# Optimization experiments

Measured on AMD Instinct MI355X. Metric: run time of the kernel, lower is better.

## Reference

```python
import jax, jax.numpy as jnp
import numpy as np
import math

B, C, H, W = 64, 32, 80, 80
HEADS, HD = 8, 4
L = H * W
INV_PI = 1.0 / math.pi


def _conv2d(x, w, pad):
    return jax.lax.conv_general_dilated(x, w, (1, 1), pad, dimension_numbers=('NCHW', 'OIHW', 'NCHW'))


def _lin_angular(x, qkv_w, proj_w, proj_b, dconv_w):
    # x: (B, L, C) -> softmax-free angular linear attention
    qkv = (x @ qkv_w.T).reshape(B, L, 3, HEADS, HD).transpose(2, 0, 3, 1, 4)
    q, k, v = qkv[0], qkv[1], qkv[2]  # (B, HEADS, L, HD)
    q = q / jnp.linalg.norm(q, axis=-1, keepdims=True)
    k = k / jnp.linalg.norm(k, axis=-1, keepdims=True)
    # depthwise conv over L with kernel (9,1), one channel per head
    dconv_v = jax.lax.conv_general_dilated(v, dconv_w, (1, 1), ((4, 4), (0, 0)),
                                           feature_group_count=HEADS,
                                           dimension_numbers=('NCHW', 'OIHW', 'NCHW'))
    attn = jnp.einsum('bhld,bhle->bhde', k, v)  # (B,H,HD,HD)
    out = 0.5 * v + INV_PI * jnp.einsum('bhld,bhde->bhle', q, attn)
    out = out / jnp.linalg.norm(out, axis=-1, keepdims=True)
    out = out + dconv_v
    out = out.transpose(0, 2, 1, 3).reshape(B, L, C)
    return out @ proj_w.T + proj_b


def _xca(x, qkv_w, temp, proj_w, proj_b):
    # x: (B, L, C) -> cross-covariance (channel) attention
    qkv = (x @ qkv_w.T).reshape(B, L, 3, HEADS, HD).transpose(2, 0, 3, 4, 1)
    q, k, v = qkv[0], qkv[1], qkv[2]  # (B, HEADS, HD, L)
    q = q / jnp.maximum(jnp.linalg.norm(q, axis=-1, keepdims=True), 1e-12)
    k = k / jnp.maximum(jnp.linalg.norm(k, axis=-1, keepdims=True), 1e-12)
    attn = jax.nn.softmax(jnp.einsum('bhdn,bhen->bhde', q, k) * temp, axis=-1)
    out = jnp.einsum('bhde,bhen->bhdn', attn, v)  # (B,H,HD,L)
    out = out.transpose(0, 3, 1, 2).reshape(B, L, C)
    return out @ proj_w.T + proj_b


def _chan_vec(f, wa, ba, wa2, ba2, wm, bm, wm2, bm2):
    # f: (B, C, L) -> (B, C, 1) pooled channel descriptor (avg + max branches)
    avg = f.mean(axis=-1)  # (B, C)
    mx = f.max(axis=-1)    # (B, C)
    a = jax.nn.relu(avg @ wa.T + ba) @ wa2.T + ba2
    m = jax.nn.relu(mx @ wm.T + bm) @ wm2.T + bm2
    return (a + m)[..., None]  # (B, C, 1)


def _spatial_gate(a, c1w, c1b, c2w, c2b):
    # a: (B, C, L) -> (B, 1, L) softmax spatial gate
    am = a.reshape(B, C, H, W)
    pooled = jnp.concatenate([am.mean(axis=1, keepdims=True), am.max(axis=1, keepdims=True)], axis=1)
    y = jax.nn.relu(_conv2d(pooled, c1w, ((1, 1), (1, 1))) + c1b[None, :, None, None])
    y = _conv2d(y, c2w, ((1, 1), (1, 1))) + c2b[None, :, None, None]
    return jax.nn.softmax(y.reshape(B, 1, L), axis=-1)


def _forward(rgb, freq, la_qkv_w, la_proj_w, la_proj_b, la_dconv_w,
             xa_qkv_w, xa_temp, xa_proj_w, xa_proj_b,
             c1s_w, c1s_b, c2s_w, c2s_b,
             avg1_w, avg1_b, max1_w, max1_b, avg2_w, avg2_b, max2_w, max2_b,
             avg11_w, avg11_b, max11_w, max11_b, avg22_w, avg22_b, max22_w, max22_b):
    x1 = rgb.reshape(B, C, L).transpose(0, 2, 1)  # to_3d: (B, L, C)
    la1 = _lin_angular(x1, la_qkv_w, la_proj_w, la_proj_b, la_dconv_w)
    x2 = freq.reshape(B, C, L).transpose(0, 2, 1)
    xa1 = _xca(x2, xa_qkv_w, xa_temp, xa_proj_w, xa_proj_b)
    # CAFM works on flattened (B, C, L)
    f1 = la1.transpose(0, 2, 1)
    f2 = xa1.transpose(0, 2, 1)
    a1 = _chan_vec(f1, avg1_w, avg1_b, avg11_w, avg11_b, max1_w, max1_b, max11_w, max11_b)
    a2 = _chan_vec(f2, avg2_w, avg2_b, avg22_w, avg22_b, max2_w, max2_b, max22_w, max22_b)
    cross = jnp.einsum('bci,bdi->bcd', a1, a2)  # (B, C, C)
    a1f = jnp.einsum('bcd,bdl->bcl', jax.nn.softmax(cross, axis=-1), f1)
    a2f = jnp.einsum('bcd,bdl->bcl', jax.nn.softmax(cross.transpose(0, 2, 1), axis=-1), f2)
    g1 = _spatial_gate(a1f, c1s_w, c1s_b, c2s_w, c2s_b)
    g2 = _spatial_gate(a2f, c1s_w, c1s_b, c2s_w, c2s_b)
    f1 = f1 * g1 + f1
    f2 = f2 * g2 + f2
    # torch: (B,C,L).transpose(0,1) -> (C,B,L); sum; permute(1,2,0) -> (B,L,C); to_4d -> (B,C,H,W)
    # transposes cancel: equivalent to (f1+f2).reshape(B, C, H, W)
    return (f1 + f2).reshape(B, C, H, W)


def setup_inputs() -> dict:
    key = jax.random.key(0)
    ks = iter(jax.random.split(key, 40))
    def rn(shape, s=0.05):
        return jax.random.normal(next(ks), shape, dtype=jnp.float32) * s
    return dict(
        rgb=jax.random.normal(next(ks), (B, C, H, W), dtype=jnp.float32),
        freq=jax.random.normal(next(ks), (B, C, H, W), dtype=jnp.float32),
        la_qkv_w=rn((3 * C, C)), la_proj_w=rn((C, C)), la_proj_b=jnp.zeros((C,), jnp.float32),
        la_dconv_w=rn((HEADS, 1, 9, 1)),
        xa_qkv_w=rn((3 * C, C)), xa_temp=jnp.ones((HEADS, 1, 1), jnp.float32),
        xa_proj_w=rn((C, C)), xa_proj_b=jnp.zeros((C,), jnp.float32),
        c1s_w=rn((1, 2, 3, 3)), c1s_b=jnp.zeros((1,), jnp.float32),
        c2s_w=rn((1, 1, 3, 3)), c2s_b=jnp.zeros((1,), jnp.float32),
        avg1_w=rn((16, C)), avg1_b=jnp.zeros((16,), jnp.float32),
        max1_w=rn((16, C)), max1_b=jnp.zeros((16,), jnp.float32),
        avg2_w=rn((16, C)), avg2_b=jnp.zeros((16,), jnp.float32),
        max2_w=rn((16, C)), max2_b=jnp.zeros((16,), jnp.float32),
        avg11_w=rn((C, 16)), avg11_b=jnp.zeros((C,), jnp.float32),
        max11_w=rn((C, 16)), max11_b=jnp.zeros((C,), jnp.float32),
        avg22_w=rn((C, 16)), avg22_b=jnp.zeros((C,), jnp.float32),
        max22_w=rn((C, 16)), max22_b=jnp.zeros((C,), jnp.float32),
    )


def reference(rgb, freq, la_qkv_w, la_proj_w, la_proj_b, la_dconv_w,
              xa_qkv_w, xa_temp, xa_proj_w, xa_proj_b,
              c1s_w, c1s_b, c2s_w, c2s_b,
              avg1_w, avg1_b, max1_w, max1_b, avg2_w, avg2_b, max2_w, max2_b,
              avg11_w, avg11_b, max11_w, max11_b, avg22_w, avg22_b, max22_w, max22_b):
    return _forward(rgb, freq, la_qkv_w, la_proj_w, la_proj_b, la_dconv_w,
                    xa_qkv_w, xa_temp, xa_proj_w, xa_proj_b,
                    c1s_w, c1s_b, c2s_w, c2s_b,
                    avg1_w, avg1_b, max1_w, max1_b, avg2_w, avg2_b, max2_w, max2_b,
                    avg11_w, avg11_b, max11_w, max11_b, avg22_w, avg22_b, max22_w, max22_b)
```

## Files before the change

### kernel.cpp

```cpp
#include <hip/hip_runtime.h>

#define BN 64
#define CN 32
#define HEADSN 8
#define HDN 4
#define LN 6400
#define CL (CN*LN)


__device__ __forceinline__ unsigned fenc(float f){
  unsigned u = __float_as_uint(f);
  return (u & 0x80000000u) ? ~u : (u | 0x80000000u);
}
__device__ __forceinline__ float fdec(unsigned u){
  unsigned v = (u & 0x80000000u) ? (u & 0x7FFFFFFFu) : ~u;
  return __uint_as_float(v);
}

__device__ __forceinline__ unsigned pk_bf16(float a, float b){
  unsigned ua = __float_as_uint(a), ub = __float_as_uint(b);
  ua = (ua + 0x7fffu + ((ua >> 16) & 1u)) >> 16;
  ub = (ub + 0x7fffu + ((ub >> 16) & 1u)) >> 16;
  return ua | (ub << 16);
}
__device__ __forceinline__ float2 upk_bf16(unsigned u){
  return make_float2(__uint_as_float(u << 16), __uint_as_float(u & 0xffff0000u));
}

template<bool MAXOP>
__device__ __forceinline__ float bfly32(const float* in, int lane, int* chOut){
  const bool h0 = (lane & 1)  != 0, h1 = (lane & 2)  != 0, h2 = (lane & 4) != 0,
             h3 = (lane & 8)  != 0, h4 = (lane & 16) != 0;
  float a[16];
  #pragma unroll
  for (int i = 0; i < 16; ++i){
    float send = h0 ? in[i] : in[i+16];
    float keep = h0 ? in[i+16] : in[i];
    float recv = __shfl_xor(send, 1, 64);
    a[i] = MAXOP ? fmaxf(keep, recv) : keep + recv;
  }
  float b[8];
  #pragma unroll
  for (int i = 0; i < 8; ++i){
    float send = h1 ? a[i] : a[i+8];
    float keep = h1 ? a[i+8] : a[i];
    float recv = __shfl_xor(send, 2, 64);
    b[i] = MAXOP ? fmaxf(keep, recv) : keep + recv;
  }
  float c[4];
  #pragma unroll
  for (int i = 0; i < 4; ++i){
    float send = h2 ? b[i] : b[i+4];
    float keep = h2 ? b[i+4] : b[i];
    float recv = __shfl_xor(send, 4, 64);
    c[i] = MAXOP ? fmaxf(keep, recv) : keep + recv;
  }
  float d[2];
  #pragma unroll
  for (int i = 0; i < 2; ++i){
    float send = h3 ? c[i] : c[i+2];
    float keep = h3 ? c[i+2] : c[i];
    float recv = __shfl_xor(send, 8, 64);
    d[i] = MAXOP ? fmaxf(keep, recv) : keep + recv;
  }
  float e;
  {
    float send = h4 ? d[0] : d[1];
    float keep = h4 ? d[1] : d[0];
    float recv = __shfl_xor(send, 16, 64);
    e = MAXOP ? fmaxf(keep, recv) : keep + recv;
  }
  {
    float recv = __shfl_xor(e, 32, 64);
    e = MAXOP ? fmaxf(e, recv) : e + recv;
  }
  *chOut = (h0?16:0)|(h1?8:0)|(h2?4:0)|(h3?2:0)|(h4?1:0);
  return e;
}

__device__ __forceinline__ float bfly16_sum(const float* in, int lane, int* chOut){
  const bool h0 = (lane & 1) != 0, h1 = (lane & 2) != 0, h2 = (lane & 4) != 0,
             h3 = (lane & 8) != 0;
  float a[8];
  #pragma unroll
  for (int i = 0; i < 8; ++i){
    float send = h0 ? in[i] : in[i+8];
    float keep = h0 ? in[i+8] : in[i];
    float recv = __shfl_xor(send, 1, 64);
    a[i] = keep + recv;
  }
  float b[4];
  #pragma unroll
  for (int i = 0; i < 4; ++i){
    float send = h1 ? a[i] : a[i+4];
    float keep = h1 ? a[i+4] : a[i];
    float recv = __shfl_xor(send, 2, 64);
    b[i] = keep + recv;
  }
  float c[2];
  #pragma unroll
  for (int i = 0; i < 2; ++i){
    float send = h2 ? b[i] : b[i+2];
    float keep = h2 ? b[i+2] : b[i];
    float recv = __shfl_xor(send, 4, 64);
    c[i] = keep + recv;
  }
  float e;
  {
    float send = h3 ? c[0] : c[1];
    float keep = h3 ? c[1] : c[0];
    float recv = __shfl_xor(send, 8, 64);
    e = keep + recv;
  }
  e += __shfl_xor(e, 16, 64);
  e += __shfl_xor(e, 32, 64);
  *chOut = (h0?8:0)|(h1?4:0)|(h2?2:0)|(h3?1:0);
  return e;
}

__global__ __launch_bounds__(256) void k_reduce2(const float* __restrict__ rgb,
    const float* __restrict__ freq, const float* __restrict__ Wla,
    const float* __restrict__ Wxa, float* __restrict__ la_attn,
    float* __restrict__ xa_sums){
  __shared__ float2 xs2[256*17];
  const bool isXA = blockIdx.x >= 25;
  const int b = blockIdx.y, tid = threadIdx.x;
  const int l0 = (isXA ? (int)blockIdx.x - 25 : (int)blockIdx.x)*256;
  const float* xg = (isXA ? freq : rgb) + (size_t)b*CL + l0;
  #pragma unroll
  for (int c2 = 0; c2 < 16; ++c2){
    float e0 = xg[(2*c2)*LN + tid];
    float e1 = xg[(2*c2+1)*LN + tid];
    xs2[tid*17 + c2] = make_float2(e0, e1);
  }
  __syncthreads();
  const int wave = __builtin_amdgcn_readfirstlane(tid >> 6);
  const int lane = tid & 63;
  if (!isXA){
    const float* Wk = Wla + (32 + wave*8)*32;
    const float* Wv = Wla + (64 + wave*8)*32;
    float acc[32];
    #pragma unroll
    for (int i = 0; i < 32; ++i) acc[i] = 0.f;
    for (int it = 0; it < 4; ++it){
      const int ll = it*64 + lane;
      float xv[32];
      #pragma unroll
      for (int c2 = 0; c2 < 16; ++c2){
        float2 t = xs2[ll*17 + c2];
        xv[2*c2] = t.x; xv[2*c2+1] = t.y;
      }
      float kk[8], vv[8];
      #pragma unroll
      for (int r = 0; r < 8; ++r){ kk[r] = 0.f; vv[r] = 0.f; }
      #pragma unroll
      for (int c = 0; c < 32; ++c){
        #pragma unroll
        for (int r = 0; r < 8; ++r){
          kk[r] = fmaf(Wk[r*32 + c], xv[c], kk[r]);
          vv[r] = fmaf(Wv[r*32 + c], xv[c], vv[r]);
        }
      }
      #pragma unroll
      for (int hh = 0; hh < 2; ++hh){
        const float* k = kk + hh*4;
        const float* v = vv + hh*4;
        float rn = rsqrtf(k[0]*k[0] + k[1]*k[1] + k[2]*k[2] + k[3]*k[3]);
        #pragma unroll
        for (int d = 0; d < 4; ++d){
          float kn = k[d]*rn;
          #pragma unroll
          for (int e = 0; e < 4; ++e)
            acc[hh*16 + d*4 + e] = fmaf(kn, v[e], acc[hh*16 + d*4 + e]);
        }
      }
    }
    int ch;
    float s = bfly32<false>(acc, lane, &ch);
    if (lane < 32) atomicAdd(la_attn + b*128 + wave*32 + ch, s);
  } else {
    const float* Wq = Wxa + (0  + wave*8)*32;
    const float* Wk = Wxa + (32 + wave*8)*32;
    float acc[48];
    #pragma unroll
    for (int i = 0; i < 48; ++i) acc[i] = 0.f;
    for (int it = 0; it < 4; ++it){
      const int ll = it*64 + lane;
      float xv[32];
      #pragma unroll
      for (int c2 = 0; c2 < 16; ++c2){
        float2 t = xs2[ll*17 + c2];
        xv[2*c2] = t.x; xv[2*c2+1] = t.y;
      }
      float qq[8], kk[8];
      #pragma unroll
      for (int r = 0; r < 8; ++r){ qq[r] = 0.f; kk[r] = 0.f; }
      #pragma unroll
      for (int c = 0; c < 32; ++c){
        #pragma unroll
        for (int r = 0; r < 8; ++r){
          qq[r] = fmaf(Wq[r*32 + c], xv[c], qq[r]);
          kk[r] = fmaf(Wk[r*32 + c], xv[c], kk[r]);
        }
      }
      #pragma unroll
      for (int hh = 0; hh < 2; ++hh){
        const float* q = qq + hh*4;
        const float* k = kk + hh*4;
        const int base = hh*24;
        #pragma unroll
        for (int d = 0; d < 4; ++d){
          #pragma unroll
          for (int e = 0; e < 4; ++e)
            acc[base + d*4 + e] = fmaf(q[d], k[e], acc[base + d*4 + e]);
        }
        #pragma unroll
        for (int d = 0; d < 4; ++d) acc[base + 16 + d] = fmaf(q[d], q[d], acc[base + 16 + d]);
        #pragma unroll
        for (int e = 0; e < 4; ++e) acc[base + 20 + e] = fmaf(k[e], k[e], acc[base + 20 + e]);
      }
    }
    float* dst = xa_sums + b*192 + wave*48;
    int ch;
    float s0 = bfly32<false>(acc, lane, &ch);
    if (lane < 32) atomicAdd(dst + ch, s0);
    int ch2;
    float s1 = bfly16_sum(acc + 32, lane, &ch2);
    if (lane < 16) atomicAdd(dst + 32 + ch2, s1);
  }
}

__global__ __launch_bounds__(64) void k_fold(const float* __restrict__ xa_sums,
                                             const float* __restrict__ temp,
                                             const float* __restrict__ Wqkv,
                                             const float* __restrict__ Wp,
                                             float* __restrict__ M2){
  __shared__ float attn_s[128];
  const int b = blockIdx.x, t = threadIdx.x;
  if (t < 32){
    const int h = t >> 2, d = t & 3;
    const float* xss = xa_sums + b*192 + h*24;
    const float tmp = temp[h];
    const float nq = fmaxf(sqrtf(xss[16 + d]), 1e-12f);
    float lg[4]; float m = -1e30f;
    #pragma unroll
    for (int e = 0; e < 4; ++e){
      float nk = fmaxf(sqrtf(xss[20 + e]), 1e-12f);
      lg[e] = xss[d*4 + e] * tmp / (nq*nk);
      m = fmaxf(m, lg[e]);
    }
    float Z = 0.f;
    #pragma unroll
    for (int e = 0; e < 4; ++e){ lg[e] = __expf(lg[e] - m); Z += lg[e]; }
    float iZ = 1.f/Z;
    #pragma unroll
    for (int e = 0; e < 4; ++e) attn_s[h*16 + d*4 + e] = lg[e]*iZ;
  }
  __syncthreads();
  if (t < 32){
    const int c = t;
    const float* Wv = Wqkv + 64*32;
    float tmpv[32];
    #pragma unroll
    for (int k = 0; k < 32; ++k){
      const int h = k >> 2, d = k & 3;
      float s = 0.f;
      #pragma unroll
      for (int e = 0; e < 4; ++e)
        s = fmaf(attn_s[h*16 + d*4 + e], Wv[(h*4 + e)*32 + c], s);
      tmpv[k] = s;
    }
    float out[32];
    #pragma unroll
    for (int r = 0; r < 32; ++r) out[r] = 0.f;
    #pragma unroll
    for (int k = 0; k < 32; ++k){
      #pragma unroll
      for (int r = 0; r < 32; ++r)
        out[r] = fmaf(Wp[r*32 + k], tmpv[k], out[r]);
    }
    #pragma unroll
    for (int r = 0; r < 32; ++r) M2[b*1024 + r*32 + c] = out[r];
  }
}

__global__ __launch_bounds__(256) void k_finalize2(const float* __restrict__ rgb,
    const float* __restrict__ freq, const float* __restrict__ Wqkv,
    const float* __restrict__ la_attn, const float* __restrict__ dconv_w,
    const float* __restrict__ Wp, const float* __restrict__ bp,
    const float* __restrict__ M2, const float* __restrict__ xbp,
    float* __restrict__ f1, float* __restrict__ sum1, unsigned* __restrict__ max1e,
    float* __restrict__ f2, float* __restrict__ sum2, unsigned* __restrict__ max2e){
  __shared__ unsigned vsh[264*17];
  const bool isXA = blockIdx.x >= 25;
  const int b = blockIdx.y, tid = threadIdx.x;
  const int l0 = (isXA ? (int)blockIdx.x - 25 : (int)blockIdx.x)*256;
  const int l = l0 + tid, lane = tid & 63;
  if (!isXA){
    const float* xg = rgb + (size_t)b*CL;
    float x[32];
    #pragma unroll
    for (int c = 0; c < 32; ++c) x[c] = xg[c*LN + l];
    {
      float v[32];
      #pragma unroll
      for (int r = 0; r < 32; ++r) v[r] = 0.f;
      const float* Wv = Wqkv + 64*32;
      #pragma unroll
      for (int c = 0; c < 32; ++c){
        #pragma unroll
        for (int r = 0; r < 32; ++r) v[r] = fmaf(Wv[r*32 + c], x[c], v[r]);
      }
      #pragma unroll
      for (int c2 = 0; c2 < 16; ++c2)
        vsh[(tid+4)*17 + c2] = pk_bf16(v[2*c2], v[2*c2+1]);
    }
    if (tid < 128){
      const int p = tid >> 4, c2 = tid & 15;
      const int hl  = (p < 4) ? (l0 - 4 + p) : (l0 + 252 + p);
      const int pos = (p < 4) ? p : (256 + p);
      float2 vh = make_float2(0.f, 0.f);
      if (hl >= 0 && hl < LN){
        const float* W0 = Wqkv + (64 + 2*c2)*32;
        #pragma unroll 8
        for (int cc = 0; cc < 32; ++cc){
          float xv = xg[cc*LN + hl];
          vh.x = fmaf(W0[cc],      xv, vh.x);
          vh.y = fmaf(W0[32 + cc], xv, vh.y);
        }
      }
      vsh[pos*17 + c2] = pk_bf16(vh.x, vh.y);
    }
    __syncthreads();
    float y[32];
    #pragma unroll
    for (int h = 0; h < 8; ++h){
      float q0 = 0.f, q1 = 0.f, q2 = 0.f, q3 = 0.f;
      const float* Wq = Wqkv + h*4*32;
      #pragma unroll
      for (int c = 0; c < 32; ++c){
        q0 = fmaf(Wq[c],      x[c], q0);
        q1 = fmaf(Wq[32 + c], x[c], q1);
        q2 = fmaf(Wq[64 + c], x[c], q2);
        q3 = fmaf(Wq[96 + c], x[c], q3);
      }
      const float rnq = rsqrtf(q0*q0 + q1*q1 + q2*q2 + q3*q3);
      q0 *= rnq; q1 *= rnq; q2 *= rnq; q3 *= rnq;
      const float* at = la_attn + b*128 + h*16;
      const float2 v01 = upk_bf16(vsh[(tid+4)*17 + h*2]);
      const float2 v23 = upk_bf16(vsh[(tid+4)*17 + h*2 + 1]);
      const float vo[4] = {v01.x, v01.y, v23.x, v23.y};
      float o[4]; float ss = 0.f;
      #pragma unroll
      for (int e = 0; e < 4; ++e){
        float t = 0.f;
        t = fmaf(q0, at[e],      t);
        t = fmaf(q1, at[4 + e],  t);
        t = fmaf(q2, at[8 + e],  t);
        t = fmaf(q3, at[12 + e], t);
        o[e] = fmaf(0.31830988618379067f, t, 0.5f*vo[e]);
        ss = fmaf(o[e], o[e], ss);
      }
      const float rno = rsqrtf(ss);
      float dc[4] = {0.f, 0.f, 0.f, 0.f};
      #pragma unroll
      for (int j = 0; j < 9; ++j){
        const float w = dconv_w[h*9 + j];
        const float2 p0 = upk_bf16(vsh[(tid + j)*17 + h*2]);
        const float2 p1 = upk_bf16(vsh[(tid + j)*17 + h*2 + 1]);
        dc[0] = fmaf(w, p0.x, dc[0]);
        dc[1] = fmaf(w, p0.y, dc[1]);
        dc[2] = fmaf(w, p1.x, dc[2]);
        dc[3] = fmaf(w, p1.y, dc[3]);
      }
      #pragma unroll
      for (int e = 0; e < 4; ++e) y[h*4 + e] = fmaf(o[e], rno, dc[e]);
    }
    float vals[32];
    float* f1p = f1 + (size_t)b*CL + l;
    #pragma unroll
    for (int r = 0; r < 32; ++r){
      float val = bp[r];
      #pragma unroll
      for (int c = 0; c < 32; ++c) val = fmaf(Wp[r*32 + c], y[c], val);
      f1p[r*LN] = val;
      vals[r] = val;
    }
    int ch;
    float s = bfly32<false>(vals, lane, &ch);
    float m = bfly32<true >(vals, lane, &ch);
    if (lane < 32){
      atomicAdd(&sum1[b*32 + ch], s);
      atomicMax(&max1e[b*32 + ch], fenc(m));
    }
  } else {
    const float* xg = freq + (size_t)b*CL;
    float x[32];
    #pragma unroll
    for (int c = 0; c < 32; ++c) x[c] = xg[c*LN + l];
    const float* M = M2 + b*1024;
    float vals[32];
    #pragma unroll
    for (int r = 0; r < 32; ++r) vals[r] = xbp[r];
    #pragma unroll
    for (int c = 0; c < 32; ++c){
      #pragma unroll
      for (int r = 0; r < 32; ++r) vals[r] = fmaf(M[r*32 + c], x[c], vals[r]);
    }
    float* f2p = f2 + (size_t)b*CL + l;
    #pragma unroll
    for (int r = 0; r < 32; ++r) f2p[r*LN] = vals[r];
    int ch;
    float s = bfly32<false>(vals, lane, &ch);
    float m = bfly32<true >(vals, lane, &ch);
    if (lane < 32){
      atomicAdd(&sum2[b*32 + ch], s);
      atomicMax(&max2e[b*32 + ch], fenc(m));
    }
  }
}

__global__ __launch_bounds__(64) void k_vec(
  const float* __restrict__ sum1, const unsigned* __restrict__ max1e,
  const float* __restrict__ sum2, const unsigned* __restrict__ max2e,
  const float* __restrict__ a1w, const float* __restrict__ a1b,
  const float* __restrict__ m1w, const float* __restrict__ m1b,
  const float* __restrict__ a2w, const float* __restrict__ a2b,
  const float* __restrict__ m2w, const float* __restrict__ m2b,
  const float* __restrict__ a11w, const float* __restrict__ a11b,
  const float* __restrict__ m11w, const float* __restrict__ m11b,
  const float* __restrict__ a22w, const float* __restrict__ a22b,
  const float* __restrict__ m22w, const float* __restrict__ m22b,
  float* __restrict__ w1o, float* __restrict__ w2o){
  __shared__ float avg1[32], mx1[32], avg2[32], mx2[32];
  __shared__ float h_a1[16], h_m1[16], h_a2[16], h_m2[16];
  __shared__ float a1v[32], a2v[32];
  const int b = blockIdx.x, t = threadIdx.x;
  if (t < 32){
    avg1[t] = sum1[b*32 + t] * (1.f/6400.f);
    mx1[t]  = fdec(max1e[b*32 + t]);
    avg2[t] = sum2[b*32 + t] * (1.f/6400.f);
    mx2[t]  = fdec(max2e[b*32 + t]);
  }
  __syncthreads();
  if (t < 16){
    float s1 = a1b[t], s2 = m1b[t], s3 = a2b[t], s4 = m2b[t];
    for (int c = 0; c < 32; ++c){
      s1 = fmaf(avg1[c], a1w[t*32 + c], s1);
      s2 = fmaf(mx1[c],  m1w[t*32 + c], s2);
      s3 = fmaf(avg2[c], a2w[t*32 + c], s3);
      s4 = fmaf(mx2[c],  m2w[t*32 + c], s4);
    }
    h_a1[t] = fmaxf(s1, 0.f); h_m1[t] = fmaxf(s2, 0.f);
    h_a2[t] = fmaxf(s3, 0.f); h_m2[t] = fmaxf(s4, 0.f);
  }
  __syncthreads();
  if (t < 32){
    float v1 = a11b[t] + m11b[t];
    float v2 = a22b[t] + m22b[t];
    for (int k = 0; k < 16; ++k){
      v1 += h_a1[k]*a11w[t*16 + k] + h_m1[k]*m11w[t*16 + k];
      v2 += h_a2[k]*a22w[t*16 + k] + h_m2[k]*m22w[t*16 + k];
    }
    a1v[t] = v1; a2v[t] = v2;
  }
  __syncthreads();
  if (t < 32){
    float s = a1v[t], m = -1e30f;
    for (int d = 0; d < 32; ++d) m = fmaxf(m, s*a2v[d]);
    float Z = 0.f;
    for (int d = 0; d < 32; ++d) Z += __expf(s*a2v[d] - m);
    float iZ = 1.f/Z;
    for (int d = 0; d < 32; ++d) w1o[b*1024 + t*32 + d] = __expf(s*a2v[d] - m)*iZ;
    float s2 = a2v[t]; m = -1e30f;
    for (int d = 0; d < 32; ++d) m = fmaxf(m, s2*a1v[d]);
    Z = 0.f;
    for (int d = 0; d < 32; ++d) Z += __expf(s2*a1v[d] - m);
    iZ = 1.f/Z;
    for (int d = 0; d < 32; ++d) w2o[b*1024 + t*32 + d] = __expf(s2*a1v[d] - m)*iZ;
  }
}

__global__ __launch_bounds__(256) void k_mix(const float* __restrict__ f1,
    const float* __restrict__ f2, const float* __restrict__ w1,
    const float* __restrict__ w2, float* __restrict__ pooled1,
    float* __restrict__ pooled2){
  const int b = blockIdx.y, l = blockIdx.x*256 + threadIdx.x;
  float fv[32], av[32];
  {
    const float* f1p = f1 + (size_t)b*CL + l;
    #pragma unroll
    for (int d = 0; d < 32; ++d) fv[d] = f1p[d*LN];
    const float* W = w1 + b*1024;
    #pragma unroll
    for (int c = 0; c < 32; ++c) av[c] = 0.f;
    #pragma unroll
    for (int d = 0; d < 32; ++d){
      #pragma unroll
      for (int c = 0; c < 32; ++c) av[c] = fmaf(W[c*32 + d], fv[d], av[c]);
    }
    float s = 0.f, m = -1e30f;
    #pragma unroll
    for (int c = 0; c < 32; ++c){ s += av[c]; m = fmaxf(m, av[c]); }
    pooled1[(size_t)b*2*LN + l]      = s*(1.f/32.f);
    pooled1[(size_t)b*2*LN + LN + l] = m;
  }
  {
    const float* f2p = f2 + (size_t)b*CL + l;
    #pragma unroll
    for (int d = 0; d < 32; ++d) fv[d] = f2p[d*LN];
    const float* W = w2 + b*1024;
    #pragma unroll
    for (int c = 0; c < 32; ++c) av[c] = 0.f;
    #pragma unroll
    for (int d = 0; d < 32; ++d){
      #pragma unroll
      for (int c = 0; c < 32; ++c) av[c] = fmaf(W[c*32 + d], fv[d], av[c]);
    }
    float s = 0.f, m = -1e30f;
    #pragma unroll
    for (int c = 0; c < 32; ++c){ s += av[c]; m = fmaxf(m, av[c]); }
    pooled2[(size_t)b*2*LN + l]      = s*(1.f/32.f);
    pooled2[(size_t)b*2*LN + LN + l] = m;
  }
}

__global__ __launch_bounds__(256) void k_gate(const float* __restrict__ pooled1,
    const float* __restrict__ pooled2, const float* __restrict__ c1w,
    const float* __restrict__ c1b, const float* __restrict__ c2w,
    const float* __restrict__ c2b, float* __restrict__ g1, float* __restrict__ g2){
  __shared__ float y1s[6400];
  __shared__ float red[8];
  const int b = blockIdx.y, t = blockIdx.x, tid = threadIdx.x;
  const float* src = (t == 0 ? pooled1 : pooled2) + (size_t)b*2*LN;
  float* dst = (t == 0 ? g1 : g2) + (size_t)b*LN;
  for (int i = tid; i < 6400; i += 256){
    const int yy = i/80, xx = i - yy*80;
    float a = c1b[0];
    #pragma unroll
    for (int ky = 0; ky < 3; ++ky){
      const int y2 = yy + ky - 1;
      if (y2 < 0 || y2 >= 80) continue;
      #pragma unroll
      for (int kx = 0; kx < 3; ++kx){
        const int x2 = xx + kx - 1;
        if (x2 < 0 || x2 >= 80) continue;
        const int j = y2*80 + x2;
        a = fmaf(src[j],        c1w[ky*3 + kx],     a);
        a = fmaf(src[6400 + j], c1w[9 + ky*3 + kx], a);
      }
    }
    y1s[i] = fmaxf(a, 0.f);
  }
  __syncthreads();
  float y2r[25]; float lmax = -1e30f;
  #pragma unroll
  for (int ii = 0; ii < 25; ++ii){
    const int i = tid + ii*256;
    const int yy = i/80, xx = i - yy*80;
    float a = c2b[0];
    #pragma unroll
    for (int ky = 0; ky < 3; ++ky){
      const int y2 = yy + ky - 1;
      if (y2 < 0 || y2 >= 80) continue;
      #pragma unroll
      for (int kx = 0; kx < 3; ++kx){
        const int x2 = xx + kx - 1;
        if (x2 < 0 || x2 >= 80) continue;
        a = fmaf(y1s[y2*80 + x2], c2w[ky*3 + kx], a);
      }
    }
    y2r[ii] = a; lmax = fmaxf(lmax, a);
  }
  #pragma unroll
  for (int off = 32; off >= 1; off >>= 1) lmax = fmaxf(lmax, __shfl_xor(lmax, off, 64));
  if ((tid & 63) == 0) red[tid >> 6] = lmax;
  __syncthreads();
  const float bmax = fmaxf(fmaxf(red[0], red[1]), fmaxf(red[2], red[3]));
  float lsum = 0.f;
  #pragma unroll
  for (int ii = 0; ii < 25; ++ii){
    float e = __expf(y2r[ii] - bmax);
    y2r[ii] = e; lsum += e;
  }
  #pragma unroll
  for (int off = 32; off >= 1; off >>= 1) lsum += __shfl_xor(lsum, off, 64);
  if ((tid & 63) == 0) red[4 + (tid >> 6)] = lsum;
  __syncthreads();
  const float inv = 1.f/(red[4] + red[5] + red[6] + red[7]);
  #pragma unroll
  for (int ii = 0; ii < 25; ++ii) dst[tid + ii*256] = y2r[ii]*inv;
}

__global__ __launch_bounds__(256) void k_final(const float* __restrict__ f1,
    const float* __restrict__ f2, const float* __restrict__ g1,
    const float* __restrict__ g2, float* __restrict__ out){
  const int i = blockIdx.x*256 + threadIdx.x;
  const int flat = i*4;
  const int b = flat / CL;
  const int rem = flat - b*CL;
  const int l = rem % LN;
  const float4 a  = *(const float4*)(f1 + flat);
  const float4 c  = *(const float4*)(f2 + flat);
  const float4 ga = *(const float4*)(g1 + b*LN + l);
  const float4 gc = *(const float4*)(g2 + b*LN + l);
  float4 o;
  o.x = fmaf(a.x, ga.x, a.x) + fmaf(c.x, gc.x, c.x);
  o.y = fmaf(a.y, ga.y, a.y) + fmaf(c.y, gc.y, c.y);
  o.z = fmaf(a.z, ga.z, a.z) + fmaf(c.z, gc.z, c.z);
  o.w = fmaf(a.w, ga.w, a.w) + fmaf(c.w, gc.w, c.w);
  *(float4*)(out + flat) = o;
}

extern "C" void kernel_launch(void* const* d_in, const int* in_sizes, int n_in,
                              void* d_out, int out_size, void* d_ws, size_t ws_size,
                              hipStream_t stream){
  const float* rgb     = (const float*)d_in[0];
  const float* freq    = (const float*)d_in[1];
  const float* la_qkv  = (const float*)d_in[2];
  const float* la_pw   = (const float*)d_in[3];
  const float* la_pb   = (const float*)d_in[4];
  const float* la_dw   = (const float*)d_in[5];
  const float* xa_qkv  = (const float*)d_in[6];
  const float* xa_temp = (const float*)d_in[7];
  const float* xa_pw   = (const float*)d_in[8];
  const float* xa_pb   = (const float*)d_in[9];
  const float* c1w     = (const float*)d_in[10];
  const float* c1b     = (const float*)d_in[11];
  const float* c2w     = (const float*)d_in[12];
  const float* c2b     = (const float*)d_in[13];

  float* ws = (float*)d_ws;
  size_t o = 0;
  float* f1      = ws + o; o += (size_t)BN*CL;
  float* f2      = ws + o; o += (size_t)BN*CL;
  float* la_attn = ws + o; o += BN*128;
  float* xa_sums = ws + o; o += BN*192;
  float* sum1    = ws + o; o += BN*32;
  unsigned* max1e = (unsigned*)(ws + o); o += BN*32;
  float* sum2    = ws + o; o += BN*32;
  unsigned* max2e = (unsigned*)(ws + o); o += BN*32;
  float* w1      = ws + o; o += BN*1024;
  float* w2      = ws + o; o += BN*1024;
  float* pooled1 = ws + o; o += (size_t)BN*2*LN;
  float* pooled2 = ws + o; o += (size_t)BN*2*LN;
  float* g1      = ws + o; o += (size_t)BN*LN;
  float* g2      = ws + o; o += (size_t)BN*LN;
  float* M2      = ws + o; o += (size_t)BN*1024;

  const size_t nz = (size_t)BN*128 + BN*192 + (size_t)BN*32*4;
  hipMemsetAsync(la_attn, 0, nz*sizeof(float), stream);

  k_reduce2<<<dim3(50, BN), 256, 0, stream>>>(rgb, freq, la_qkv, xa_qkv, la_attn, xa_sums);
  k_fold   <<<BN, 64, 0, stream>>>(xa_sums, xa_temp, xa_qkv, xa_pw, M2);
  k_finalize2<<<dim3(50, BN), 256, 0, stream>>>(rgb, freq, la_qkv, la_attn, la_dw,
                                                la_pw, la_pb, M2, xa_pb,
                                                f1, sum1, max1e, f2, sum2, max2e);
  k_vec<<<BN, 64, 0, stream>>>(sum1, max1e, sum2, max2e,
      (const float*)d_in[14], (const float*)d_in[15], (const float*)d_in[16], (const float*)d_in[17],
      (const float*)d_in[18], (const float*)d_in[19], (const float*)d_in[20], (const float*)d_in[21],
      (const float*)d_in[22], (const float*)d_in[23], (const float*)d_in[24], (const float*)d_in[25],
      (const float*)d_in[26], (const float*)d_in[27], (const float*)d_in[28], (const float*)d_in[29],
      w1, w2);
  k_mix  <<<dim3(25, BN), 256, 0, stream>>>(f1, f2, w1, w2, pooled1, pooled2);
  k_gate <<<dim3(2, BN), 256, 0, stream>>>(pooled1, pooled2, c1w, c1b, c2w, c2b, g1, g2);
  k_final<<<12800, 256, 0, stream>>>(f1, f2, g1, g2, (float*)d_out);
}
```

Measured before the change: 537.5 us.

## Fuse fold and channel-vector kernels into consumers; use 512-thread blocks

Folds the small k_fold work (XCA softmax and the M2 projection matrix) into the XCA blocks of k_finalize2. It also folds k_vec's channel-weight computation into each k_mix block, keeping the weights in shared memory. This removes two tiny launches and their global round-trips. k_reduce2 and k_finalize2 move to 512-thread blocks that each handle two tiles. The trade-off is redundant per-block recomputation of the fold and vector work: every XCA finalize block and every mix block recomputes its batch's matrices serially on 32 threads, which adds latency before the main work starts.

```diff
diff --git a/kernel.cpp b/kernel.cpp
--- a/kernel.cpp
+++ b/kernel.cpp
@@ -118,23 +118,32 @@
   return e;
 }
 
-__global__ __launch_bounds__(256) void k_reduce2(const float* __restrict__ rgb,
+__global__ __launch_bounds__(512) void k_reduce2(const float* __restrict__ rgb,
     const float* __restrict__ freq, const float* __restrict__ Wla,
     const float* __restrict__ Wxa, float* __restrict__ la_attn,
     float* __restrict__ xa_sums){
-  __shared__ float2 xs2[256*17];
+  __shared__ float2 xs2[2*128*17];
   const bool isXA = blockIdx.x >= 25;
   const int b = blockIdx.y, tid = threadIdx.x;
-  const int l0 = (isXA ? (int)blockIdx.x - 25 : (int)blockIdx.x)*256;
+  const int half = tid >> 8;
+  const int wt = tid & 255;
+  const int bxt = isXA ? (int)blockIdx.x - 25 : (int)blockIdx.x;
+  const int l0 = (bxt*2 + half)*128;
   const float* xg = (isXA ? freq : rgb) + (size_t)b*CL + l0;
-  #pragma unroll
-  for (int c2 = 0; c2 < 16; ++c2){
-    float e0 = xg[(2*c2)*LN + tid];
-    float e1 = xg[(2*c2+1)*LN + tid];
-    xs2[tid*17 + c2] = make_float2(e0, e1);
-  }
-  __syncthreads();
-  const int wave = __builtin_amdgcn_readfirstlane(tid >> 6);
+  float2* xs = xs2 + half*(128*17);
+  {
+    const int px = wt & 127;
+    const int c2b_ = (wt >> 7)*8;
+    #pragma unroll
+    for (int j = 0; j < 8; ++j){
+      const int c2 = c2b_ + j;
+      float e0 = xg[(2*c2)*LN + px];
+      float e1 = xg[(2*c2+1)*LN + px];
+      xs[px*17 + c2] = make_float2(e0, e1);
+    }
+  }
+  __syncthreads();
+  const int wave = __builtin_amdgcn_readfirstlane((tid >> 6) & 3);
   const int lane = tid & 63;
   if (!isXA){
     const float* Wk = Wla + (32 + wave*8)*32;
@@ -142,12 +151,12 @@
     float acc[32];
     #pragma unroll
     for (int i = 0; i < 32; ++i) acc[i] = 0.f;
-    for (int it = 0; it < 4; ++it){
+    for (int it = 0; it < 2; ++it){
       const int ll = it*64 + lane;
       float xv[32];
       #pragma unroll
       for (int c2 = 0; c2 < 16; ++c2){
-        float2 t = xs2[ll*17 + c2];
+        float2 t = xs[ll*17 + c2];
         xv[2*c2] = t.x; xv[2*c2+1] = t.y;
       }
       float kk[8], vv[8];
@@ -184,12 +193,12 @@
     float acc[48];
     #pragma unroll
     for (int i = 0; i < 48; ++i) acc[i] = 0.f;
-    for (int it = 0; it < 4; ++it){
+    for (int it = 0; it < 2; ++it){
       const int ll = it*64 + lane;
       float xv[32];
       #pragma unroll
       for (int c2 = 0; c2 < 16; ++c2){
-        float2 t = xs2[ll*17 + c2];
+        float2 t = xs[ll*17 + c2];
         xv[2*c2] = t.x; xv[2*c2+1] = t.y;
       }
       float qq[8], kk[8];
@@ -230,274 +239,276 @@
   }
 }
 
-__global__ __launch_bounds__(64) void k_fold(const float* __restrict__ xa_sums,
-                                             const float* __restrict__ temp,
-                                             const float* __restrict__ Wqkv,
-                                             const float* __restrict__ Wp,
-                                             float* __restrict__ M2){
-  __shared__ float attn_s[128];
-  const int b = blockIdx.x, t = threadIdx.x;
-  if (t < 32){
-    const int h = t >> 2, d = t & 3;
-    const float* xss = xa_sums + b*192 + h*24;
-    const float tmp = temp[h];
-    const float nq = fmaxf(sqrtf(xss[16 + d]), 1e-12f);
-    float lg[4]; float m = -1e30f;
-    #pragma unroll
-    for (int e = 0; e < 4; ++e){
-      float nk = fmaxf(sqrtf(xss[20 + e]), 1e-12f);
-      lg[e] = xss[d*4 + e] * tmp / (nq*nk);
-      m = fmaxf(m, lg[e]);
-    }
-    float Z = 0.f;
-    #pragma unroll
-    for (int e = 0; e < 4; ++e){ lg[e] = __expf(lg[e] - m); Z += lg[e]; }
-    float iZ = 1.f/Z;
-    #pragma unroll
-    for (int e = 0; e < 4; ++e) attn_s[h*16 + d*4 + e] = lg[e]*iZ;
-  }
-  __syncthreads();
-  if (t < 32){
-    const int c = t;
-    const float* Wv = Wqkv + 64*32;
-    float tmpv[32];
-    #pragma unroll
-    for (int k = 0; k < 32; ++k){
-      const int h = k >> 2, d = k & 3;
-      float s = 0.f;
-      #pragma unroll
-      for (int e = 0; e < 4; ++e)
-        s = fmaf(attn_s[h*16 + d*4 + e], Wv[(h*4 + e)*32 + c], s);
-      tmpv[k] = s;
-    }
-    float out[32];
-    #pragma unroll
-    for (int r = 0; r < 32; ++r) out[r] = 0.f;
-    #pragma unroll
-    for (int k = 0; k < 32; ++k){
-      #pragma unroll
-      for (int r = 0; r < 32; ++r)
-        out[r] = fmaf(Wp[r*32 + k], tmpv[k], out[r]);
-    }
-    #pragma unroll
-    for (int r = 0; r < 32; ++r) M2[b*1024 + r*32 + c] = out[r];
-  }
-}
-
-__global__ __launch_bounds__(256) void k_finalize2(const float* __restrict__ rgb,
+__global__ __launch_bounds__(512) void k_finalize2(const float* __restrict__ rgb,
     const float* __restrict__ freq, const float* __restrict__ Wqkv,
     const float* __restrict__ la_attn, const float* __restrict__ dconv_w,
     const float* __restrict__ Wp, const float* __restrict__ bp,
-    const float* __restrict__ M2, const float* __restrict__ xbp,
+    const float* __restrict__ Wxa, const float* __restrict__ xtemp,
+    const float* __restrict__ xWp, const float* __restrict__ xbp,
+    const float* __restrict__ xa_sums,
     float* __restrict__ f1, float* __restrict__ sum1, unsigned* __restrict__ max1e,
     float* __restrict__ f2, float* __restrict__ sum2, unsigned* __restrict__ max2e){
-  __shared__ unsigned vsh[264*17];
-  const bool isXA = blockIdx.x >= 25;
+  __shared__ unsigned vsh[2*264*17];
+  const bool isXA = blockIdx.x >= 13;
   const int b = blockIdx.y, tid = threadIdx.x;
-  const int l0 = (isXA ? (int)blockIdx.x - 25 : (int)blockIdx.x)*256;
-  const int l = l0 + tid, lane = tid & 63;
+  const int half = tid >> 8, t = tid & 255;
+  const int bxt = isXA ? (int)blockIdx.x - 13 : (int)blockIdx.x;
+  const int tile = bxt*2 + half;
+  const bool valid = tile < 25;
+  const int l0 = tile*256;
+  const int l = l0 + t, lane = tid & 63;
+  unsigned* vs = vsh + half*(264*17);
   if (!isXA){
     const float* xg = rgb + (size_t)b*CL;
     float x[32];
-    #pragma unroll
-    for (int c = 0; c < 32; ++c) x[c] = xg[c*LN + l];
-    {
-      float v[32];
-      #pragma unroll
-      for (int r = 0; r < 32; ++r) v[r] = 0.f;
-      const float* Wv = Wqkv + 64*32;
+    if (valid){
+      #pragma unroll
+      for (int c = 0; c < 32; ++c) x[c] = xg[c*LN + l];
+      {
+        float v[32];
+        #pragma unroll
+        for (int r = 0; r < 32; ++r) v[r] = 0.f;
+        const float* Wv = Wqkv + 64*32;
+        #pragma unroll
+        for (int c = 0; c < 32; ++c){
+          #pragma unroll
+          for (int r = 0; r < 32; ++r) v[r] = fmaf(Wv[r*32 + c], x[c], v[r]);
+        }
+        #pragma unroll
+        for (int c2 = 0; c2 < 16; ++c2)
+          vs[(t+4)*17 + c2] = pk_bf16(v[2*c2], v[2*c2+1]);
+      }
+      if (t < 128){
+        const int p = t >> 4, c2 = t & 15;
+        const int hl  = (p < 4) ? (l0 - 4 + p) : (l0 + 252 + p);
+        const int pos = (p < 4) ? p : (256 + p);
+        float2 vh = make_float2(0.f, 0.f);
+        if (hl >= 0 && hl < LN){
+          const float* W0 = Wqkv + (64 + 2*c2)*32;
+          #pragma unroll 8
+          for (int cc = 0; cc < 32; ++cc){
+            float xv = xg[cc*LN + hl];
+            vh.x = fmaf(W0[cc],      xv, vh.x);
+            vh.y = fmaf(W0[32 + cc], xv, vh.y);
+          }
+        }
+        vs[pos*17 + c2] = pk_bf16(vh.x, vh.y);
+      }
+    }
+    __syncthreads();
+    if (valid){
+      float y[32];
+      #pragma unroll
+      for (int h = 0; h < 8; ++h){
+        float q0 = 0.f, q1 = 0.f, q2 = 0.f, q3 = 0.f;
+        const float* Wq = Wqkv + h*4*32;
+        #pragma unroll
+        for (int c = 0; c < 32; ++c){
+          q0 = fmaf(Wq[c],      x[c], q0);
+          q1 = fmaf(Wq[32 + c], x[c], q1);
+          q2 = fmaf(Wq[64 + c], x[c], q2);
+          q3 = fmaf(Wq[96 + c], x[c], q3);
+        }
+        const float rnq = rsqrtf(q0*q0 + q1*q1 + q2*q2 + q3*q3);
+        q0 *= rnq; q1 *= rnq; q2 *= rnq; q3 *= rnq;
+        const float* at = la_attn + b*128 + h*16;
+        const float2 v01 = upk_bf16(vs[(t+4)*17 + h*2]);
+        const float2 v23 = upk_bf16(vs[(t+4)*17 + h*2 + 1]);
+        const float vo[4] = {v01.x, v01.y, v23.x, v23.y};
+        float o[4]; float ss = 0.f;
+        #pragma unroll
+        for (int e = 0; e < 4; ++e){
+          float tt = 0.f;
+          tt = fmaf(q0, at[e],      tt);
+          tt = fmaf(q1, at[4 + e],  tt);
+          tt = fmaf(q2, at[8 + e],  tt);
+          tt = fmaf(q3, at[12 + e], tt);
+          o[e] = fmaf(0.31830988618379067f, tt, 0.5f*vo[e]);
+          ss = fmaf(o[e], o[e], ss);
+        }
+        const float rno = rsqrtf(ss);
+        float dc[4] = {0.f, 0.f, 0.f, 0.f};
+        #pragma unroll
+        for (int j = 0; j < 9; ++j){
+          const float w = dconv_w[h*9 + j];
+          const float2 p0 = upk_bf16(vs[(t + j)*17 + h*2]);
+          const float2 p1 = upk_bf16(vs[(t + j)*17 + h*2 + 1]);
+          dc[0] = fmaf(w, p0.x, dc[0]);
+          dc[1] = fmaf(w, p0.y, dc[1]);
+          dc[2] = fmaf(w, p1.x, dc[2]);
+          dc[3] = fmaf(w, p1.y, dc[3]);
+        }
+        #pragma unroll
+        for (int e = 0; e < 4; ++e) y[h*4 + e] = fmaf(o[e], rno, dc[e]);
+      }
+      float vals[32];
+      float* f1p = f1 + (size_t)b*CL + l;
+      #pragma unroll
+      for (int r = 0; r < 32; ++r){
+        float val = bp[r];
+        #pragma unroll
+        for (int c = 0; c < 32; ++c) val = fmaf(Wp[r*32 + c], y[c], val);
+        f1p[r*LN] = val;
+        vals[r] = val;
+      }
+      int ch;
+      float s = bfly32<false>(vals, lane, &ch);
+      float m = bfly32<true >(vals, lane, &ch);
+      if (lane < 32){
+        atomicAdd(&sum1[b*32 + ch], s);
+        atomicMax(&max1e[b*32 + ch], fenc(m));
+      }
+    }
+  } else {
+    float* M2s    = (float*)vsh;
+    float* attn_s = ((float*)vsh) + 1024;
+    if (tid < 32){
+      const int h = tid >> 2, d = tid & 3;
+      const float* xss = xa_sums + b*192 + h*24;
+      const float tmp = xtemp[h];
+      const float nq = fmaxf(sqrtf(xss[16 + d]), 1e-12f);
+      float lg[4]; float m = -1e30f;
+      #pragma unroll
+      for (int e = 0; e < 4; ++e){
+        float nk = fmaxf(sqrtf(xss[20 + e]), 1e-12f);
+        lg[e] = xss[d*4 + e] * tmp / (nq*nk);
+        m = fmaxf(m, lg[e]);
+      }
+      float Z = 0.f;
+      #pragma unroll
+      for (int e = 0; e < 4; ++e){ lg[e] = __expf(lg[e] - m); Z += lg[e]; }
+      float iZ = 1.f/Z;
+      #pragma unroll
+      for (int e = 0; e < 4; ++e) attn_s[h*16 + d*4 + e] = lg[e]*iZ;
+    }
+    __syncthreads();
+    if (tid < 32){
+      const int c = tid;
+      const float* Wv = Wxa + 64*32;
+      float tmpv[32];
+      #pragma unroll
+      for (int k = 0; k < 32; ++k){
+        const int h = k >> 2, d = k & 3;
+        float s = 0.f;
+        #pragma unroll
+        for (int e = 0; e < 4; ++e)
+          s = fmaf(attn_s[h*16 + d*4 + e], Wv[(h*4 + e)*32 + c], s);
+        tmpv[k] = s;
+      }
+      float out[32];
+      #pragma unroll
+      for (int r = 0; r < 32; ++r) out[r] = 0.f;
+      #pragma unroll
+      for (int k = 0; k < 32; ++k){
+        #pragma unroll
+        for (int r = 0; r < 32; ++r)
+          out[r] = fmaf(xWp[r*32 + k], tmpv[k], out[r]);
+      }
+      #pragma unroll
+      for (int r = 0; r < 32; ++r) M2s[r*32 + c] = out[r];
+    }
+    __syncthreads();
+    if (valid){
+      const float* xg = freq + (size_t)b*CL;
+      float x[32];
+      #pragma unroll
+      for (int c = 0; c < 32; ++c) x[c] = xg[c*LN + l];
+      float vals[32];
+      #pragma unroll
+      for (int r = 0; r < 32; ++r) vals[r] = xbp[r];
       #pragma unroll
       for (int c = 0; c < 32; ++c){
         #pragma unroll
-        for (int r = 0; r < 32; ++r) v[r] = fmaf(Wv[r*32 + c], x[c], v[r]);
-      }
-      #pragma unroll
-      for (int c2 = 0; c2 < 16; ++c2)
-        vsh[(tid+4)*17 + c2] = pk_bf16(v[2*c2], v[2*c2+1]);
-    }
-    if (tid < 128){
-      const int p = tid >> 4, c2 = tid & 15;
-      const int hl  = (p < 4) ? (l0 - 4 + p) : (l0 + 252 + p);
-      const int pos = (p < 4) ? p : (256 + p);
-      float2 vh = make_float2(0.f, 0.f);
-      if (hl >= 0 && hl < LN){
-        const float* W0 = Wqkv + (64 + 2*c2)*32;
-        #pragma unroll 8
-        for (int cc = 0; cc < 32; ++cc){
-          float xv = xg[cc*LN + hl];
-          vh.x = fmaf(W0[cc],      xv, vh.x);
-          vh.y = fmaf(W0[32 + cc], xv, vh.y);
-        }
-      }
-      vsh[pos*17 + c2] = pk_bf16(vh.x, vh.y);
-    }
-    __syncthreads();
-    float y[32];
-    #pragma unroll
-    for (int h = 0; h < 8; ++h){
-      float q0 = 0.f, q1 = 0.f, q2 = 0.f, q3 = 0.f;
-      const float* Wq = Wqkv + h*4*32;
-      #pragma unroll
-      for (int c = 0; c < 32; ++c){
-        q0 = fmaf(Wq[c],      x[c], q0);
-        q1 = fmaf(Wq[32 + c], x[c], q1);
-        q2 = fmaf(Wq[64 + c], x[c], q2);
-        q3 = fmaf(Wq[96 + c], x[c], q3);
-      }
-      const float rnq = rsqrtf(q0*q0 + q1*q1 + q2*q2 + q3*q3);
-      q0 *= rnq; q1 *= rnq; q2 *= rnq; q3 *= rnq;
-      const float* at = la_attn + b*128 + h*16;
-      const float2 v01 = upk_bf16(vsh[(tid+4)*17 + h*2]);
-      const float2 v23 = upk_bf16(vsh[(tid+4)*17 + h*2 + 1]);
-      const float vo[4] = {v01.x, v01.y, v23.x, v23.y};
-      float o[4]; float ss = 0.f;
-      #pragma unroll
-      for (int e = 0; e < 4; ++e){
-        float t = 0.f;
-        t = fmaf(q0, at[e],      t);
-        t = fmaf(q1, at[4 + e],  t);
-        t = fmaf(q2, at[8 + e],  t);
-        t = fmaf(q3, at[12 + e], t);
-        o[e] = fmaf(0.31830988618379067f, t, 0.5f*vo[e]);
-        ss = fmaf(o[e], o[e], ss);
-      }
-      const float rno = rsqrtf(ss);
-      float dc[4] = {0.f, 0.f, 0.f, 0.f};
-      #pragma unroll
-      for (int j = 0; j < 9; ++j){
-        const float w = dconv_w[h*9 + j];
-        const float2 p0 = upk_bf16(vsh[(tid + j)*17 + h*2]);
-        const float2 p1 = upk_bf16(vsh[(tid + j)*17 + h*2 + 1]);
-        dc[0] = fmaf(w, p0.x, dc[0]);
-        dc[1] = fmaf(w, p0.y, dc[1]);
-        dc[2] = fmaf(w, p1.x, dc[2]);
-        dc[3] = fmaf(w, p1.y, dc[3]);
-      }
-      #pragma unroll
-      for (int e = 0; e < 4; ++e) y[h*4 + e] = fmaf(o[e], rno, dc[e]);
-    }
-    float vals[32];
-    float* f1p = f1 + (size_t)b*CL + l;
-    #pragma unroll
-    for (int r = 0; r < 32; ++r){
-      float val = bp[r];
-      #pragma unroll
-      for (int c = 0; c < 32; ++c) val = fmaf(Wp[r*32 + c], y[c], val);
-      f1p[r*LN] = val;
-      vals[r] = val;
-    }
-    int ch;
-    float s = bfly32<false>(vals, lane, &ch);
-    float m = bfly32<true >(vals, lane, &ch);
-    if (lane < 32){
-      atomicAdd(&sum1[b*32 + ch], s);
-      atomicMax(&max1e[b*32 + ch], fenc(m));
-    }
-  } else {
-    const float* xg = freq + (size_t)b*CL;
-    float x[32];
-    #pragma unroll
-    for (int c = 0; c < 32; ++c) x[c] = xg[c*LN + l];
-    const float* M = M2 + b*1024;
-    float vals[32];
-    #pragma unroll
-    for (int r = 0; r < 32; ++r) vals[r] = xbp[r];
-    #pragma unroll
-    for (int c = 0; c < 32; ++c){
-      #pragma unroll
-      for (int r = 0; r < 32; ++r) vals[r] = fmaf(M[r*32 + c], x[c], vals[r]);
-    }
-    float* f2p = f2 + (size_t)b*CL + l;
-    #pragma unroll
-    for (int r = 0; r < 32; ++r) f2p[r*LN] = vals[r];
-    int ch;
-    float s = bfly32<false>(vals, lane, &ch);
-    float m = bfly32<true >(vals, lane, &ch);
-    if (lane < 32){
-      atomicAdd(&sum2[b*32 + ch], s);
-      atomicMax(&max2e[b*32 + ch], fenc(m));
-    }
-  }
-}
-
-__global__ __launch_bounds__(64) void k_vec(
-  const float* __restrict__ sum1, const unsigned* __restrict__ max1e,
-  const float* __restrict__ sum2, const unsigned* __restrict__ max2e,
-  const float* __restrict__ a1w, const float* __restrict__ a1b,
-  const float* __restrict__ m1w, const float* __restrict__ m1b,
-  const float* __restrict__ a2w, const float* __restrict__ a2b,
-  const float* __restrict__ m2w, const float* __restrict__ m2b,
-  const float* __restrict__ a11w, const float* __restrict__ a11b,
-  const float* __restrict__ m11w, const float* __restrict__ m11b,
-  const float* __restrict__ a22w, const float* __restrict__ a22b,
-  const float* __restrict__ m22w, const float* __restrict__ m22b,
-  float* __restrict__ w1o, float* __restrict__ w2o){
+        for (int r = 0; r < 32; ++r) vals[r] = fmaf(M2s[r*32 + c], x[c], vals[r]);
+      }
+      float* f2p = f2 + (size_t)b*CL + l;
+      #pragma unroll
+      for (int r = 0; r < 32; ++r) f2p[r*LN] = vals[r];
+      int ch;
+      float s = bfly32<false>(vals, lane, &ch);
+      float m = bfly32<true >(vals, lane, &ch);
+      if (lane < 32){
+        atomicAdd(&sum2[b*32 + ch], s);
+        atomicMax(&max2e[b*32 + ch], fenc(m));
+      }
+    }
+  }
+}
+
+__global__ __launch_bounds__(256) void k_mix(const float* __restrict__ f1,
+    const float* __restrict__ f2,
+    const float* __restrict__ sum1, const unsigned* __restrict__ max1e,
+    const float* __restrict__ sum2, const unsigned* __restrict__ max2e,
+    const float* __restrict__ a1w, const float* __restrict__ a1b,
+    const float* __restrict__ m1w, const float* __restrict__ m1b,
+    const float* __restrict__ a2w, const float* __restrict__ a2b,
+    const float* __restrict__ m2w, const float* __restrict__ m2b,
+    const float* __restrict__ a11w, const float* __restrict__ a11b,
+    const float* __restrict__ m11w, const float* __restrict__ m11b,
+    const float* __restrict__ a22w, const float* __restrict__ a22b,
+    const float* __restrict__ m22w, const float* __restrict__ m22b,
+    float* __restrict__ pooled1, float* __restrict__ pooled2){
   __shared__ float avg1[32], mx1[32], avg2[32], mx2[32];
   __shared__ float h_a1[16], h_m1[16], h_a2[16], h_m2[16];
   __shared__ float a1v[32], a2v[32];
-  const int b = blockIdx.x, t = threadIdx.x;
-  if (t < 32){
-    avg1[t] = sum1[b*32 + t] * (1.f/6400.f);
-    mx1[t]  = fdec(max1e[b*32 + t]);
-    avg2[t] = sum2[b*32 + t] * (1.f/6400.f);
-    mx2[t]  = fdec(max2e[b*32 + t]);
-  }
-  __syncthreads();
-  if (t < 16){
-    float s1 = a1b[t], s2 = m1b[t], s3 = a2b[t], s4 = m2b[t];
+  __shared__ float w1s[1024], w2s[1024];
+  const int b = blockIdx.y, tid = threadIdx.x;
+  const int l = blockIdx.x*256 + tid;
+  if (tid < 32){
+    avg1[tid] = sum1[b*32 + tid] * (1.f/6400.f);
+    mx1[tid]  = fdec(max1e[b*32 + tid]);
+    avg2[tid] = sum2[b*32 + tid] * (1.f/6400.f);
+    mx2[tid]  = fdec(max2e[b*32 + tid]);
+  }
+  __syncthreads();
+  if (tid < 16){
+    float s1 = a1b[tid], s2 = m1b[tid], s3 = a2b[tid], s4 = m2b[tid];
     for (int c = 0; c < 32; ++c){
-      s1 = fmaf(avg1[c], a1w[t*32 + c], s1);
-      s2 = fmaf(mx1[c],  m1w[t*32 + c], s2);
-      s3 = fmaf(avg2[c], a2w[t*32 + c], s3);
-      s4 = fmaf(mx2[c],  m2w[t*32 + c], s4);
-    }
-    h_a1[t] = fmaxf(s1, 0.f); h_m1[t] = fmaxf(s2, 0.f);
-    h_a2[t] = fmaxf(s3, 0.f); h_m2[t] = fmaxf(s4, 0.f);
-  }
-  __syncthreads();
-  if (t < 32){
-    float v1 = a11b[t] + m11b[t];
-    float v2 = a22b[t] + m22b[t];
+      s1 = fmaf(avg1[c], a1w[tid*32 + c], s1);
+      s2 = fmaf(mx1[c],  m1w[tid*32 + c], s2);
+      s3 = fmaf(avg2[c], a2w[tid*32 + c], s3);
+      s4 = fmaf(mx2[c],  m2w[tid*32 + c], s4);
+    }
+    h_a1[tid] = fmaxf(s1, 0.f); h_m1[tid] = fmaxf(s2, 0.f);
+    h_a2[tid] = fmaxf(s3, 0.f); h_m2[tid] = fmaxf(s4, 0.f);
+  }
+  __syncthreads();
+  if (tid < 32){
+    float v1 = a11b[tid] + m11b[tid];
+    float v2 = a22b[tid] + m22b[tid];
     for (int k = 0; k < 16; ++k){
-      v1 += h_a1[k]*a11w[t*16 + k] + h_m1[k]*m11w[t*16 + k];
-      v2 += h_a2[k]*a22w[t*16 + k] + h_m2[k]*m22w[t*16 + k];
-    }
-    a1v[t] = v1; a2v[t] = v2;
-  }
-  __syncthreads();
-  if (t < 32){
-    float s = a1v[t], m = -1e30f;
+      v1 += h_a1[k]*a11w[tid*16 + k] + h_m1[k]*m11w[tid*16 + k];
+      v2 += h_a2[k]*a22w[tid*16 + k] + h_m2[k]*m22w[tid*16 + k];
+    }
+    a1v[tid] = v1; a2v[tid] = v2;
+  }
+  __syncthreads();
+  if (tid < 32){
+    float s = a1v[tid], m = -1e30f;
     for (int d = 0; d < 32; ++d) m = fmaxf(m, s*a2v[d]);
     float Z = 0.f;
     for (int d = 0; d < 32; ++d) Z += __expf(s*a2v[d] - m);
     float iZ = 1.f/Z;
-    for (int d = 0; d < 32; ++d) w1o[b*1024 + t*32 + d] = __expf(s*a2v[d] - m)*iZ;
-    float s2 = a2v[t]; m = -1e30f;
+    for (int d = 0; d < 32; ++d) w1s[tid*32 + d] = __expf(s*a2v[d] - m)*iZ;
+    float s2 = a2v[tid]; m = -1e30f;
     for (int d = 0; d < 32; ++d) m = fmaxf(m, s2*a1v[d]);
     Z = 0.f;
     for (int d = 0; d < 32; ++d) Z += __expf(s2*a1v[d] - m);
     iZ = 1.f/Z;
-    for (int d = 0; d < 32; ++d) w2o[b*1024 + t*32 + d] = __expf(s2*a1v[d] - m)*iZ;
-  }
-}
-
-__global__ __launch_bounds__(256) void k_mix(const float* __restrict__ f1,
-    const float* __restrict__ f2, const float* __restrict__ w1,
-    const float* __restrict__ w2, float* __restrict__ pooled1,
-    float* __restrict__ pooled2){
-  const int b = blockIdx.y, l = blockIdx.x*256 + threadIdx.x;
+    for (int d = 0; d < 32; ++d) w2s[tid*32 + d] = __expf(s2*a1v[d] - m)*iZ;
+  }
+  __syncthreads();
   float fv[32], av[32];
   {
     const float* f1p = f1 + (size_t)b*CL + l;
     #pragma unroll
     for (int d = 0; d < 32; ++d) fv[d] = f1p[d*LN];
-    const float* W = w1 + b*1024;
     #pragma unroll
     for (int c = 0; c < 32; ++c) av[c] = 0.f;
     #pragma unroll
     for (int d = 0; d < 32; ++d){
       #pragma unroll
-      for (int c = 0; c < 32; ++c) av[c] = fmaf(W[c*32 + d], fv[d], av[c]);
+      for (int c = 0; c < 32; ++c) av[c] = fmaf(w1s[c*32 + d], fv[d], av[c]);
     }
     float s = 0.f, m = -1e30f;
     #pragma unroll
@@ -509,13 +520,12 @@
     const float* f2p = f2 + (size_t)b*CL + l;
     #pragma unroll
     for (int d = 0; d < 32; ++d) fv[d] = f2p[d*LN];
-    const float* W = w2 + b*1024;
     #pragma unroll
     for (int c = 0; c < 32; ++c) av[c] = 0.f;
     #pragma unroll
     for (int d = 0; d < 32; ++d){
       #pragma unroll
-      for (int c = 0; c < 32; ++c) av[c] = fmaf(W[c*32 + d], fv[d], av[c]);
+      for (int c = 0; c < 32; ++c) av[c] = fmaf(w2s[c*32 + d], fv[d], av[c]);
     }
     float s = 0.f, m = -1e30f;
     #pragma unroll
@@ -640,29 +650,25 @@
   unsigned* max1e = (unsigned*)(ws + o); o += BN*32;
   float* sum2    = ws + o; o += BN*32;
   unsigned* max2e = (unsigned*)(ws + o); o += BN*32;
-  float* w1      = ws + o; o += BN*1024;
-  float* w2      = ws + o; o += BN*1024;
   float* pooled1 = ws + o; o += (size_t)BN*2*LN;
   float* pooled2 = ws + o; o += (size_t)BN*2*LN;
   float* g1      = ws + o; o += (size_t)BN*LN;
   float* g2      = ws + o; o += (size_t)BN*LN;
-  float* M2      = ws + o; o += (size_t)BN*1024;
 
   const size_t nz = (size_t)BN*128 + BN*192 + (size_t)BN*32*4;
   hipMemsetAsync(la_attn, 0, nz*sizeof(float), stream);
 
-  k_reduce2<<<dim3(50, BN), 256, 0, stream>>>(rgb, freq, la_qkv, xa_qkv, la_attn, xa_sums);
-  k_fold   <<<BN, 64, 0, stream>>>(xa_sums, xa_temp, xa_qkv, xa_pw, M2);
-  k_finalize2<<<dim3(50, BN), 256, 0, stream>>>(rgb, freq, la_qkv, la_attn, la_dw,
-                                                la_pw, la_pb, M2, xa_pb,
+  k_reduce2  <<<dim3(50, BN), 512, 0, stream>>>(rgb, freq, la_qkv, xa_qkv, la_attn, xa_sums);
+  k_finalize2<<<dim3(26, BN), 512, 0, stream>>>(rgb, freq, la_qkv, la_attn, la_dw,
+                                                la_pw, la_pb,
+                                                xa_qkv, xa_temp, xa_pw, xa_pb, xa_sums,
                                                 f1, sum1, max1e, f2, sum2, max2e);
-  k_vec<<<BN, 64, 0, stream>>>(sum1, max1e, sum2, max2e,
+  k_mix  <<<dim3(25, BN), 256, 0, stream>>>(f1, f2, sum1, max1e, sum2, max2e,
       (const float*)d_in[14], (const float*)d_in[15], (const float*)d_in[16], (const float*)d_in[17],
       (const float*)d_in[18], (const float*)d_in[19], (const float*)d_in[20], (const float*)d_in[21],
       (const float*)d_in[22], (const float*)d_in[23], (const float*)d_in[24], (const float*)d_in[25],
       (const float*)d_in[26], (const float*)d_in[27], (const float*)d_in[28], (const float*)d_in[29],
-      w1, w2);
-  k_mix  <<<dim3(25, BN), 256, 0, stream>>>(f1, f2, w1, w2, pooled1, pooled2);
+      pooled1, pooled2);
   k_gate <<<dim3(2, BN), 256, 0, stream>>>(pooled1, pooled2, c1w, c1b, c2w, c2b, g1, g2);
   k_final<<<12800, 256, 0, stream>>>(f1, f2, g1, g2, (float*)d_out);
 }
```

After: 529.7 us. About the same (-1.4%).
